# Optimization experiments

Hardware: AMD Instinct MI355X
Metric: run time of the kernel (lower is better)

The kernel has to match this reference:

```python
import jax, jax.numpy as jnp
import numpy as np


def _chamfer(src, tgt):
    # src: [B, N, 3], tgt: [B, M, 3]
    x2 = jnp.sum(src * src, axis=-1)              # [B, N]
    y2 = jnp.sum(tgt * tgt, axis=-1)              # [B, M]
    xy = jnp.einsum('bnd,bmd->bnm', src, tgt)     # [B, N, M]
    d2 = x2[:, :, None] + y2[:, None, :] - 2.0 * xy
    d2 = jnp.maximum(d2, 0.0)                     # guard tiny negatives
    cham_x = jnp.min(d2, axis=2)                  # [B, N] min over tgt
    cham_y = jnp.min(d2, axis=1)                  # [B, M] min over src
    # point_reduction='mean', batch_reduction='sum'
    loss = jnp.sum(jnp.mean(cham_x, axis=1)) + jnp.sum(jnp.mean(cham_y, axis=1))
    return loss


def setup_inputs() -> dict:
    key = jax.random.key(0)
    k1, k2 = jax.random.split(key)
    src = jax.random.normal(k1, (16, 4096, 3), dtype=jnp.float32)
    tgt = jax.random.normal(k2, (16, 4096, 3), dtype=jnp.float32)
    return {"src": src, "tgt": tgt}


def reference(src, tgt):
    wgeo = 1.0
    return wgeo * _chamfer(src, tgt)
```

## Files before the change

kernel.cpp:

```cpp
#include <hip/hip_runtime.h>
#include <hip/hip_bf16.h>


#define BATCH   16
#define NPTS    4096
#define NSTRIPS 32
#define NH      2
#define COLS_PB 2048
#define CHUNKC  512
#define NCHUNKS (COLS_PB / CHUNKC)
#define NSTEP   (CHUNKC / 64)

typedef __attribute__((ext_vector_type(8)))  short short8;
typedef __attribute__((ext_vector_type(16))) float float16;

union U4S8 { uint4 u; short8 s; };

__device__ inline unsigned int bfb(float v) {
    __hip_bfloat16 h = __float2bfloat16(v);
    unsigned short u; __builtin_memcpy(&u, &h, 2);
    return (unsigned int)u;
}
__device__ inline float bff(float v) { return __bfloat162float(__float2bfloat16(v)); }

#define ONEB 0x3F80u

__device__ inline void buildA(float x, float y, float z, uint4& w0, uint4& w1) {
    float xhf = bff(x), yhf = bff(y), zhf = bff(z);
    float f = fmaf(x, x, fmaf(y, y, z * z));
    float fhf = bff(f);
    unsigned xh = bfb(xhf), yh = bfb(yhf), zh = bfb(zhf);
    unsigned xl = bfb(x - xhf), yl = bfb(y - yhf), zl = bfb(z - zhf);
    unsigned fh = bfb(fhf), fl = bfb(f - fhf);
    w0 = make_uint4(xh | (yh << 16), zh | (xh << 16),
                    yh | (zh << 16), xl | (yl << 16));
    w1 = make_uint4(zl | (fh << 16), fl | (ONEB << 16), ONEB, 0u);
}

__device__ inline void buildB(float x, float y, float z, uint4& w0, uint4& w1) {
    float xhf = bff(x), yhf = bff(y), zhf = bff(z);
    float f = fmaf(x, x, fmaf(y, y, z * z));
    float fhf = bff(f);
    unsigned a = bfb(-2.0f * xhf), b = bfb(-2.0f * yhf), c = bfb(-2.0f * zhf);
    unsigned d = bfb(-2.0f * (x - xhf)), e = bfb(-2.0f * (y - yhf)),
             g = bfb(-2.0f * (z - zhf));
    unsigned fh = bfb(fhf), fl = bfb(f - fhf);
    w0 = make_uint4(a | (b << 16), c | (d << 16),
                    e | (g << 16), a | (b << 16));
    w1 = make_uint4(c | (ONEB << 16), ONEB | (fh << 16), fl, 0u);
}

__device__ inline float tree16(const float16& a) {
    float m0 = fminf(fminf(a[0],  a[1]),  a[2]);
    float m1 = fminf(fminf(a[3],  a[4]),  a[5]);
    float m2 = fminf(fminf(a[6],  a[7]),  a[8]);
    float m3 = fminf(fminf(a[9],  a[10]), a[11]);
    float m4 = fminf(fminf(a[12], a[13]), a[14]);
    float p0 = fminf(fminf(m0, m1), a[15]);
    float p1 = fminf(fminf(m2, m3), m4);
    return fminf(p0, p1);
}

__global__ __launch_bounds__(256, 4) void chamfer_main(
    const float* __restrict__ src, const float* __restrict__ tgt,
    unsigned* __restrict__ wsC, unsigned* __restrict__ wsR)
{
    __shared__ uint4 sbuf[2][2][CHUNKC];
    __shared__ unsigned colpart[COLS_PB];

    int blk = blockIdx.x;
    const int strip = blk & (NSTRIPS - 1); blk >>= 5;
    const int b     = blk & 15;            blk >>= 4;
    const int q     = blk;
    const int qoff  = q * COLS_PB;

    const int t    = threadIdx.x;
    const int lane = t & 63;
    const int w    = t >> 6;
    const int h    = lane >> 5;
    const int l5   = lane & 31;

    const float* Araw = src + (size_t)b * NPTS * 3;
    const float* Braw = tgt + (size_t)b * NPTS * 3;

    short8 afr;
    {
        int row = strip * 128 + w * 32 + l5;
        uint4 w0, w1;
        buildA(Araw[3 * row], Araw[3 * row + 1], Araw[3 * row + 2], w0, w1);
        U4S8 tt; tt.u = h ? w1 : w0;
        afr = tt.s;
    }

#pragma unroll
    for (int i = 0; i < COLS_PB / 256; i++) colpart[t + i * 256] = 0xFFFFFFFFu;

    float nx[2][3];
    auto loadRaw = [&](int c) {
#pragma unroll
        for (int k = 0; k < 2; k++) {
            int p = qoff + c * CHUNKC + t + k * 256;
            nx[k][0] = Braw[3 * p + 0];
            nx[k][1] = Braw[3 * p + 1];
            nx[k][2] = Braw[3 * p + 2];
        }
    };
    auto convertWrite = [&](int bi) {
#pragma unroll
        for (int k = 0; k < 2; k++) {
            int lp = t + k * 256;
            uint4 w0, w1;
            buildB(nx[k][0], nx[k][1], nx[k][2], w0, w1);
            sbuf[bi][0][lp] = w0;
            sbuf[bi][1][lp] = w1;
        }
    };

    const float16 z16 = {0.f,0.f,0.f,0.f,0.f,0.f,0.f,0.f,
                         0.f,0.f,0.f,0.f,0.f,0.f,0.f,0.f};
    float rm[16];
#pragma unroll
    for (int r = 0; r < 16; r++) rm[r] = 1e30f;

    loadRaw(0);
    convertWrite(0);
    for (int c = 0; c < NCHUNKS; c++) {
        __syncthreads();
        if (c + 1 < NCHUNKS) loadRaw(c + 1);
        const int bi = c & 1;

        U4S8 c0, c1, n0, n1;
        c0.u = sbuf[bi][h][l5];
        c1.u = sbuf[bi][h][32 + l5];
#pragma unroll 4
        for (int j2 = 0; j2 < NSTEP; j2++) {
            int nj = (j2 + 1) & (NSTEP - 1);
            n0.u = sbuf[bi][h][nj * 64 + l5];
            n1.u = sbuf[bi][h][nj * 64 + 32 + l5];
            float16 a0 = __builtin_amdgcn_mfma_f32_32x32x16_bf16(afr, c0.s, z16, 0, 0, 0);
            float16 a1 = __builtin_amdgcn_mfma_f32_32x32x16_bf16(afr, c1.s, z16, 0, 0, 0);
#pragma unroll
            for (int r = 0; r < 16; r++)
                rm[r] = fminf(fminf(a0[r], a1[r]), rm[r]);
            float cm0 = tree16(a0);
            float cm1 = tree16(a1);
            const int col = c * CHUNKC + j2 * 64 + l5;
            atomicMin(&colpart[col],      __float_as_uint(fmaxf(cm0, 0.0f)));
            atomicMin(&colpart[col + 32], __float_as_uint(fmaxf(cm1, 0.0f)));
            c0 = n0; c1 = n1;
        }
        if (c + 1 < NCHUNKS) convertWrite((c + 1) & 1);
    }

    __syncthreads();
#pragma unroll
    for (int i = 0; i < COLS_PB / 256; i++) {
        const int idx = t + i * 256;
        atomicMin(&wsC[(size_t)b * NPTS + qoff + idx], colpart[idx]);
    }

#pragma unroll
    for (int mask = 1; mask <= 16; mask <<= 1)
#pragma unroll
        for (int r = 0; r < 16; r++)
            rm[r] = fminf(rm[r], __shfl_xor(rm[r], mask, 64));

    __syncthreads();
    if (l5 == 0) {
#pragma unroll
        for (int r = 0; r < 16; r++) {
            const int row = w * 32 + (r & 3) + 8 * (r >> 2) + 4 * h;
            colpart[row] = __float_as_uint(fmaxf(rm[r], 0.0f));
        }
    }
    __syncthreads();
    if (t < 128)
        atomicMin(&wsR[(size_t)b * NPTS + strip * 128 + t], colpart[t]);
}

__global__ __launch_bounds__(256) void finish_reduce(
    const unsigned* __restrict__ wsC, const unsigned* __restrict__ wsR,
    float* __restrict__ out)
{
    __shared__ float wsum[4];
    const int b = blockIdx.x;
    float v = 0.0f;
#pragma unroll
    for (int i = 0; i < 16; i++)
        v += __uint_as_float(wsC[(size_t)b * NPTS + threadIdx.x + i * 256]);
#pragma unroll
    for (int i = 0; i < 16; i++)
        v += __uint_as_float(wsR[(size_t)b * NPTS + threadIdx.x + i * 256]);
#pragma unroll
    for (int mask = 1; mask <= 32; mask <<= 1) v += __shfl_xor(v, mask, 64);
    if ((threadIdx.x & 63) == 0) wsum[threadIdx.x >> 6] = v;
    __syncthreads();
    if (threadIdx.x == 0)
        atomicAdd(out, (wsum[0] + wsum[1] + wsum[2] + wsum[3]) * (1.0f / (float)NPTS));
}

extern "C" void kernel_launch(void* const* d_in, const int* in_sizes, int n_in,
                              void* d_out, int out_size, void* d_ws, size_t ws_size,
                              hipStream_t stream)
{
    const float* src = (const float*)d_in[0];
    const float* tgt = (const float*)d_in[1];
    float* out = (float*)d_out;
    unsigned* wsC = (unsigned*)d_ws;
    unsigned* wsR = wsC + (size_t)BATCH * NPTS;

    hipMemsetAsync(out, 0, sizeof(float), stream);
    hipMemsetAsync(d_ws, 0xFF, (size_t)2 * BATCH * NPTS * sizeof(unsigned), stream);
    chamfer_main <<<NH * BATCH * NSTRIPS, 256, 0, stream>>>(src, tgt, wsC, wsR);
    finish_reduce<<<BATCH, 256, 0, stream>>>(wsC, wsR, out);
}
```

Baseline: 78.67 us.

## Tile two row groups per wave and drop chunked pipeline and output memset

Each block now covers 256 source rows (two A fragments per wave) against 1024 target columns loaded into LDS in one step. Each B fragment read from LDS feeds four MFMAs instead of two, and the column minimum is merged across both row groups before each LDS atomic, halving column atomics per MFMA. The chunked double-buffered staging loop is removed. The finish kernel becomes a single 1024-thread block that writes the output directly, so the output memset and global atomicAdd go away. The trade-offs are more accumulator registers, fewer blocks (1024 rather than 1024, same count but different shape), and a serial single-block final reduction.

```diff
diff --git a/kernel.cpp b/kernel.cpp
--- a/kernel.cpp
+++ b/kernel.cpp
@@ -4,12 +4,10 @@
 
 #define BATCH   16
 #define NPTS    4096
-#define NSTRIPS 32
-#define NH      2
-#define COLS_PB 2048
-#define CHUNKC  512
-#define NCHUNKS (COLS_PB / CHUNKC)
-#define NSTEP   (CHUNKC / 64)
+#define NSTRIPS 16
+#define NQ      4
+#define COLS_PB 1024
+#define NSTEP   (COLS_PB / 64)
 
 typedef __attribute__((ext_vector_type(8)))  short short8;
 typedef __attribute__((ext_vector_type(16))) float float16;
@@ -65,11 +63,11 @@
     const float* __restrict__ src, const float* __restrict__ tgt,
     unsigned* __restrict__ wsC, unsigned* __restrict__ wsR)
 {
-    __shared__ uint4 sbuf[2][2][CHUNKC];
+    __shared__ uint4 sbuf[2][COLS_PB];
     __shared__ unsigned colpart[COLS_PB];
 
     int blk = blockIdx.x;
-    const int strip = blk & (NSTRIPS - 1); blk >>= 5;
+    const int strip = blk & (NSTRIPS - 1); blk >>= 4;
     const int b     = blk & 15;            blk >>= 4;
     const int q     = blk;
     const int qoff  = q * COLS_PB;
@@ -83,73 +81,78 @@
     const float* Araw = src + (size_t)b * NPTS * 3;
     const float* Braw = tgt + (size_t)b * NPTS * 3;
 
-    short8 afr;
-    {
-        int row = strip * 128 + w * 32 + l5;
+    float nx[4][3];
+#pragma unroll
+    for (int k = 0; k < 4; k++) {
+        int p = qoff + t + k * 256;
+        nx[k][0] = Braw[3 * p + 0];
+        nx[k][1] = Braw[3 * p + 1];
+        nx[k][2] = Braw[3 * p + 2];
+    }
+
+    short8 afr[2];
+#pragma unroll
+    for (int g = 0; g < 2; g++) {
+        int row = strip * 256 + g * 128 + w * 32 + l5;
         uint4 w0, w1;
         buildA(Araw[3 * row], Araw[3 * row + 1], Araw[3 * row + 2], w0, w1);
         U4S8 tt; tt.u = h ? w1 : w0;
-        afr = tt.s;
+        afr[g] = tt.s;
     }
 
 #pragma unroll
     for (int i = 0; i < COLS_PB / 256; i++) colpart[t + i * 256] = 0xFFFFFFFFu;
 
-    float nx[2][3];
-    auto loadRaw = [&](int c) {
-#pragma unroll
-        for (int k = 0; k < 2; k++) {
-            int p = qoff + c * CHUNKC + t + k * 256;
-            nx[k][0] = Braw[3 * p + 0];
-            nx[k][1] = Braw[3 * p + 1];
-            nx[k][2] = Braw[3 * p + 2];
-        }
-    };
-    auto convertWrite = [&](int bi) {
-#pragma unroll
-        for (int k = 0; k < 2; k++) {
-            int lp = t + k * 256;
-            uint4 w0, w1;
-            buildB(nx[k][0], nx[k][1], nx[k][2], w0, w1);
-            sbuf[bi][0][lp] = w0;
-            sbuf[bi][1][lp] = w1;
-        }
-    };
+#pragma unroll
+    for (int k = 0; k < 4; k++) {
+        int lp = t + k * 256;
+        uint4 w0, w1;
+        buildB(nx[k][0], nx[k][1], nx[k][2], w0, w1);
+        sbuf[0][lp] = w0;
+        sbuf[1][lp] = w1;
+    }
+    __syncthreads();
 
     const float16 z16 = {0.f,0.f,0.f,0.f,0.f,0.f,0.f,0.f,
                          0.f,0.f,0.f,0.f,0.f,0.f,0.f,0.f};
-    float rm[16];
-#pragma unroll
-    for (int r = 0; r < 16; r++) rm[r] = 1e30f;
-
-    loadRaw(0);
-    convertWrite(0);
-    for (int c = 0; c < NCHUNKS; c++) {
-        __syncthreads();
-        if (c + 1 < NCHUNKS) loadRaw(c + 1);
-        const int bi = c & 1;
-
-        U4S8 c0, c1, n0, n1;
-        c0.u = sbuf[bi][h][l5];
-        c1.u = sbuf[bi][h][32 + l5];
+    float rm[2][16];
+#pragma unroll
+    for (int g = 0; g < 2; g++)
+#pragma unroll
+        for (int r = 0; r < 16; r++) rm[g][r] = 1e30f;
+
+    U4S8 c0, c1, n0, n1;
+    c0.u = sbuf[h][l5];
+    c1.u = sbuf[h][32 + l5];
 #pragma unroll 4
-        for (int j2 = 0; j2 < NSTEP; j2++) {
-            int nj = (j2 + 1) & (NSTEP - 1);
-            n0.u = sbuf[bi][h][nj * 64 + l5];
-            n1.u = sbuf[bi][h][nj * 64 + 32 + l5];
-            float16 a0 = __builtin_amdgcn_mfma_f32_32x32x16_bf16(afr, c0.s, z16, 0, 0, 0);
-            float16 a1 = __builtin_amdgcn_mfma_f32_32x32x16_bf16(afr, c1.s, z16, 0, 0, 0);
+    for (int j = 0; j < NSTEP; j++) {
+        int nj = (j + 1) & (NSTEP - 1);
+        n0.u = sbuf[h][nj * 64 + l5];
+        n1.u = sbuf[h][nj * 64 + 32 + l5];
+
+        float t0, t1;
+        {
+            float16 a0 = __builtin_amdgcn_mfma_f32_32x32x16_bf16(afr[0], c0.s, z16, 0, 0, 0);
+            float16 a1 = __builtin_amdgcn_mfma_f32_32x32x16_bf16(afr[0], c1.s, z16, 0, 0, 0);
 #pragma unroll
             for (int r = 0; r < 16; r++)
-                rm[r] = fminf(fminf(a0[r], a1[r]), rm[r]);
-            float cm0 = tree16(a0);
-            float cm1 = tree16(a1);
-            const int col = c * CHUNKC + j2 * 64 + l5;
-            atomicMin(&colpart[col],      __float_as_uint(fmaxf(cm0, 0.0f)));
-            atomicMin(&colpart[col + 32], __float_as_uint(fmaxf(cm1, 0.0f)));
-            c0 = n0; c1 = n1;
+                rm[0][r] = fminf(fminf(a0[r], a1[r]), rm[0][r]);
+            t0 = tree16(a0);
+            t1 = tree16(a1);
         }
-        if (c + 1 < NCHUNKS) convertWrite((c + 1) & 1);
+        {
+            float16 a0 = __builtin_amdgcn_mfma_f32_32x32x16_bf16(afr[1], c0.s, z16, 0, 0, 0);
+            float16 a1 = __builtin_amdgcn_mfma_f32_32x32x16_bf16(afr[1], c1.s, z16, 0, 0, 0);
+#pragma unroll
+            for (int r = 0; r < 16; r++)
+                rm[1][r] = fminf(fminf(a0[r], a1[r]), rm[1][r]);
+            t0 = fminf(t0, tree16(a0));
+            t1 = fminf(t1, tree16(a1));
+        }
+        const int col = j * 64 + l5;
+        atomicMin(&colpart[col],      __float_as_uint(fmaxf(t0, 0.0f)));
+        atomicMin(&colpart[col + 32], __float_as_uint(fmaxf(t1, 0.0f)));
+        c0 = n0; c1 = n1;
     }
 
     __syncthreads();
@@ -162,41 +165,44 @@
 #pragma unroll
     for (int mask = 1; mask <= 16; mask <<= 1)
 #pragma unroll
-        for (int r = 0; r < 16; r++)
-            rm[r] = fminf(rm[r], __shfl_xor(rm[r], mask, 64));
+        for (int g = 0; g < 2; g++)
+#pragma unroll
+            for (int r = 0; r < 16; r++)
+                rm[g][r] = fminf(rm[g][r], __shfl_xor(rm[g][r], mask, 64));
 
     __syncthreads();
     if (l5 == 0) {
 #pragma unroll
-        for (int r = 0; r < 16; r++) {
-            const int row = w * 32 + (r & 3) + 8 * (r >> 2) + 4 * h;
-            colpart[row] = __float_as_uint(fmaxf(rm[r], 0.0f));
-        }
-    }
-    __syncthreads();
-    if (t < 128)
-        atomicMin(&wsR[(size_t)b * NPTS + strip * 128 + t], colpart[t]);
-}
-
-__global__ __launch_bounds__(256) void finish_reduce(
-    const unsigned* __restrict__ wsC, const unsigned* __restrict__ wsR,
-    float* __restrict__ out)
+        for (int g = 0; g < 2; g++)
+#pragma unroll
+            for (int r = 0; r < 16; r++) {
+                const int row = g * 128 + w * 32 + (r & 3) + 8 * (r >> 2) + 4 * h;
+                colpart[row] = __float_as_uint(fmaxf(rm[g][r], 0.0f));
+            }
+    }
+    __syncthreads();
+    atomicMin(&wsR[(size_t)b * NPTS + strip * 256 + t], colpart[t]);
+}
+
+__global__ __launch_bounds__(1024) void finish_reduce(
+    const unsigned* __restrict__ ws, float* __restrict__ out)
 {
-    __shared__ float wsum[4];
-    const int b = blockIdx.x;
+    __shared__ float wsum[16];
+    const int t = threadIdx.x;
     float v = 0.0f;
 #pragma unroll
-    for (int i = 0; i < 16; i++)
-        v += __uint_as_float(wsC[(size_t)b * NPTS + threadIdx.x + i * 256]);
-#pragma unroll
-    for (int i = 0; i < 16; i++)
-        v += __uint_as_float(wsR[(size_t)b * NPTS + threadIdx.x + i * 256]);
+    for (int i = 0; i < 2 * BATCH * NPTS / 1024; i++)
+        v += __uint_as_float(ws[t + i * 1024]);
 #pragma unroll
     for (int mask = 1; mask <= 32; mask <<= 1) v += __shfl_xor(v, mask, 64);
-    if ((threadIdx.x & 63) == 0) wsum[threadIdx.x >> 6] = v;
-    __syncthreads();
-    if (threadIdx.x == 0)
-        atomicAdd(out, (wsum[0] + wsum[1] + wsum[2] + wsum[3]) * (1.0f / (float)NPTS));
+    if ((t & 63) == 0) wsum[t >> 6] = v;
+    __syncthreads();
+    if (t < 64) {
+        float s = (t < 16) ? wsum[t] : 0.0f;
+#pragma unroll
+        for (int mask = 1; mask <= 8; mask <<= 1) s += __shfl_xor(s, mask, 64);
+        if (t == 0) out[0] = s * (1.0f / (float)NPTS);
+    }
 }
 
 extern "C" void kernel_launch(void* const* d_in, const int* in_sizes, int n_in,
@@ -209,8 +215,7 @@
     unsigned* wsC = (unsigned*)d_ws;
     unsigned* wsR = wsC + (size_t)BATCH * NPTS;
 
-    hipMemsetAsync(out, 0, sizeof(float), stream);
     hipMemsetAsync(d_ws, 0xFF, (size_t)2 * BATCH * NPTS * sizeof(unsigned), stream);
-    chamfer_main <<<NH * BATCH * NSTRIPS, 256, 0, stream>>>(src, tgt, wsC, wsR);
-    finish_reduce<<<BATCH, 256, 0, stream>>>(wsC, wsR, out);
-}
+    chamfer_main <<<NQ * BATCH * NSTRIPS, 256, 0, stream>>>(src, tgt, wsC, wsR);
+    finish_reduce<<<1, 1024, 0, stream>>>(wsC, out);
+}
```

Result: slower. 113.7 us (+44.5%).

## Cut LDS atomics via cross-half shuffle; use LDS transpose for row-min; widen finish grid

Applied to the files above, without the earlier changes.

In the inner loop, the two wave halves now combine their column minima with one cross-lane shuffle, and only half the lanes issue the shared-memory atomicMin, halving the LDS atomic traffic. The row-min epilogue replaces the 5-round shuffle butterfly over 16 registers with a write to a swizzled shared buffer (reusing sbuf) followed by a 32-element scan per row. The finish kernel now uses 32 blocks that each stride over the whole workspace instead of 16 blocks, one per batch. The cost is extra shuffles in the hot loop and idle lanes during the atomics.

```diff
diff --git a/kernel.cpp b/kernel.cpp
--- a/kernel.cpp
+++ b/kernel.cpp
@@ -5,7 +5,7 @@
 #define BATCH   16
 #define NPTS    4096
 #define NSTRIPS 32
-#define NH      2
+#define NQ      2
 #define COLS_PB 2048
 #define CHUNKC  512
 #define NCHUNKS (COLS_PB / CHUNKC)
@@ -65,7 +65,7 @@
     const float* __restrict__ src, const float* __restrict__ tgt,
     unsigned* __restrict__ wsC, unsigned* __restrict__ wsR)
 {
-    __shared__ uint4 sbuf[2][2][CHUNKC];
+    __shared__ uint4    sbuf[2][2][CHUNKC];
     __shared__ unsigned colpart[COLS_PB];
 
     int blk = blockIdx.x;
@@ -133,8 +133,8 @@
         c0.u = sbuf[bi][h][l5];
         c1.u = sbuf[bi][h][32 + l5];
 #pragma unroll 4
-        for (int j2 = 0; j2 < NSTEP; j2++) {
-            int nj = (j2 + 1) & (NSTEP - 1);
+        for (int j = 0; j < NSTEP; j++) {
+            int nj = (j + 1) & (NSTEP - 1);
             n0.u = sbuf[bi][h][nj * 64 + l5];
             n1.u = sbuf[bi][h][nj * 64 + 32 + l5];
             float16 a0 = __builtin_amdgcn_mfma_f32_32x32x16_bf16(afr, c0.s, z16, 0, 0, 0);
@@ -144,53 +144,53 @@
                 rm[r] = fminf(fminf(a0[r], a1[r]), rm[r]);
             float cm0 = tree16(a0);
             float cm1 = tree16(a1);
-            const int col = c * CHUNKC + j2 * 64 + l5;
-            atomicMin(&colpart[col],      __float_as_uint(fmaxf(cm0, 0.0f)));
-            atomicMin(&colpart[col + 32], __float_as_uint(fmaxf(cm1, 0.0f)));
+            cm0 = fminf(cm0, __shfl_xor(cm0, 32, 64));
+            cm1 = fminf(cm1, __shfl_xor(cm1, 32, 64));
+            if (h == 0) {
+                const int col = c * CHUNKC + j * 64 + l5;
+                atomicMin(&colpart[col],      __float_as_uint(fmaxf(cm0, 0.0f)));
+                atomicMin(&colpart[col + 32], __float_as_uint(fmaxf(cm1, 0.0f)));
+            }
             c0 = n0; c1 = n1;
         }
         if (c + 1 < NCHUNKS) convertWrite((c + 1) & 1);
     }
 
     __syncthreads();
+
 #pragma unroll
     for (int i = 0; i < COLS_PB / 256; i++) {
         const int idx = t + i * 256;
         atomicMin(&wsC[(size_t)b * NPTS + qoff + idx], colpart[idx]);
     }
 
-#pragma unroll
-    for (int mask = 1; mask <= 16; mask <<= 1)
-#pragma unroll
-        for (int r = 0; r < 16; r++)
-            rm[r] = fminf(rm[r], __shfl_xor(rm[r], mask, 64));
-
+    float* rowbuf = (float*)&sbuf[0][0][0];
+#pragma unroll
+    for (int r = 0; r < 16; r++) {
+        const int rl = (r & 3) + 8 * (r >> 2) + 4 * h;
+        rowbuf[(w * 32 + rl) * 32 + (l5 ^ rl)] = rm[r];
+    }
     __syncthreads();
-    if (l5 == 0) {
-#pragma unroll
-        for (int r = 0; r < 16; r++) {
-            const int row = w * 32 + (r & 3) + 8 * (r >> 2) + 4 * h;
-            colpart[row] = __float_as_uint(fmaxf(rm[r], 0.0f));
-        }
-    }
-    __syncthreads();
-    if (t < 128)
-        atomicMin(&wsR[(size_t)b * NPTS + strip * 128 + t], colpart[t]);
+    if (t < 128) {
+        const int rl = t & 31;
+        float m = 1e30f;
+#pragma unroll
+        for (int cc = 0; cc < 32; cc++)
+            m = fminf(m, rowbuf[t * 32 + (cc ^ rl)]);
+        atomicMin(&wsR[(size_t)b * NPTS + strip * 128 + t],
+                  __float_as_uint(fmaxf(m, 0.0f)));
+    }
 }
 
 __global__ __launch_bounds__(256) void finish_reduce(
-    const unsigned* __restrict__ wsC, const unsigned* __restrict__ wsR,
-    float* __restrict__ out)
+    const unsigned* __restrict__ ws, float* __restrict__ out)
 {
     __shared__ float wsum[4];
-    const int b = blockIdx.x;
+    const int tg = blockIdx.x * 256 + threadIdx.x;
     float v = 0.0f;
 #pragma unroll
     for (int i = 0; i < 16; i++)
-        v += __uint_as_float(wsC[(size_t)b * NPTS + threadIdx.x + i * 256]);
-#pragma unroll
-    for (int i = 0; i < 16; i++)
-        v += __uint_as_float(wsR[(size_t)b * NPTS + threadIdx.x + i * 256]);
+        v += __uint_as_float(ws[tg + i * 8192]);
 #pragma unroll
     for (int mask = 1; mask <= 32; mask <<= 1) v += __shfl_xor(v, mask, 64);
     if ((threadIdx.x & 63) == 0) wsum[threadIdx.x >> 6] = v;
@@ -211,6 +211,6 @@
 
     hipMemsetAsync(out, 0, sizeof(float), stream);
     hipMemsetAsync(d_ws, 0xFF, (size_t)2 * BATCH * NPTS * sizeof(unsigned), stream);
-    chamfer_main <<<NH * BATCH * NSTRIPS, 256, 0, stream>>>(src, tgt, wsC, wsR);
-    finish_reduce<<<BATCH, 256, 0, stream>>>(wsC, wsR, out);
-}
+    chamfer_main <<<NQ * BATCH * NSTRIPS, 256, 0, stream>>>(src, tgt, wsC, wsR);
+    finish_reduce<<<32, 256, 0, stream>>>((const unsigned*)d_ws, out);
+}
```

Result: slower. 216.1 us (+174.7%).

## Replace global atomicMin partials with plain stores and strip-wise final reduction

Applied to the files above, without the earlier changes.

Each block now writes its per-strip column minima and per-half row minima to private workspace slots with plain stores instead of global atomicMin. The memset of the workspace is dropped. finish_reduce runs 8x more blocks, each reducing the 32 strip partials per column and the 2 row partials. This removes global atomic contention and the memset launch, at the cost of a larger workspace (about 8 MB of column partials) that the finisher must read back.

```diff
diff --git a/kernel.cpp b/kernel.cpp
--- a/kernel.cpp
+++ b/kernel.cpp
@@ -5,7 +5,7 @@
 #define BATCH   16
 #define NPTS    4096
 #define NSTRIPS 32
-#define NH      2
+#define NQ      2
 #define COLS_PB 2048
 #define CHUNKC  512
 #define NCHUNKS (COLS_PB / CHUNKC)
@@ -65,7 +65,7 @@
     const float* __restrict__ src, const float* __restrict__ tgt,
     unsigned* __restrict__ wsC, unsigned* __restrict__ wsR)
 {
-    __shared__ uint4 sbuf[2][2][CHUNKC];
+    __shared__ uint4    sbuf[2][2][CHUNKC];
     __shared__ unsigned colpart[COLS_PB];
 
     int blk = blockIdx.x;
@@ -133,8 +133,8 @@
         c0.u = sbuf[bi][h][l5];
         c1.u = sbuf[bi][h][32 + l5];
 #pragma unroll 4
-        for (int j2 = 0; j2 < NSTEP; j2++) {
-            int nj = (j2 + 1) & (NSTEP - 1);
+        for (int j = 0; j < NSTEP; j++) {
+            int nj = (j + 1) & (NSTEP - 1);
             n0.u = sbuf[bi][h][nj * 64 + l5];
             n1.u = sbuf[bi][h][nj * 64 + 32 + l5];
             float16 a0 = __builtin_amdgcn_mfma_f32_32x32x16_bf16(afr, c0.s, z16, 0, 0, 0);
@@ -144,7 +144,7 @@
                 rm[r] = fminf(fminf(a0[r], a1[r]), rm[r]);
             float cm0 = tree16(a0);
             float cm1 = tree16(a1);
-            const int col = c * CHUNKC + j2 * 64 + l5;
+            const int col = c * CHUNKC + j * 64 + l5;
             atomicMin(&colpart[col],      __float_as_uint(fmaxf(cm0, 0.0f)));
             atomicMin(&colpart[col + 32], __float_as_uint(fmaxf(cm1, 0.0f)));
             c0 = n0; c1 = n1;
@@ -153,10 +153,12 @@
     }
 
     __syncthreads();
-#pragma unroll
-    for (int i = 0; i < COLS_PB / 256; i++) {
-        const int idx = t + i * 256;
-        atomicMin(&wsC[(size_t)b * NPTS + qoff + idx], colpart[idx]);
+
+    {
+        unsigned* cdst = wsC + ((size_t)b * NSTRIPS + strip) * NPTS + qoff;
+#pragma unroll
+        for (int i = 0; i < COLS_PB / 256; i++)
+            cdst[t + i * 256] = colpart[t + i * 256];
     }
 
 #pragma unroll
@@ -175,7 +177,7 @@
     }
     __syncthreads();
     if (t < 128)
-        atomicMin(&wsR[(size_t)b * NPTS + strip * 128 + t], colpart[t]);
+        wsR[((size_t)q * BATCH + b) * NPTS + strip * 128 + t] = colpart[t];
 }
 
 __global__ __launch_bounds__(256) void finish_reduce(
@@ -183,19 +185,29 @@
     float* __restrict__ out)
 {
     __shared__ float wsum[4];
-    const int b = blockIdx.x;
+    const int b   = blockIdx.x >> 3;
+    const int seg = blockIdx.x & 7;
+    const int t   = threadIdx.x;
+
     float v = 0.0f;
 #pragma unroll
-    for (int i = 0; i < 16; i++)
-        v += __uint_as_float(wsC[(size_t)b * NPTS + threadIdx.x + i * 256]);
-#pragma unroll
-    for (int i = 0; i < 16; i++)
-        v += __uint_as_float(wsR[(size_t)b * NPTS + threadIdx.x + i * 256]);
+    for (int cc = 0; cc < 2; cc++) {
+        const int idx = seg * 512 + cc * 256 + t;
+        const unsigned* base = wsC + (size_t)b * NSTRIPS * NPTS + idx;
+        unsigned m = base[0];
+#pragma unroll 8
+        for (int s = 1; s < NSTRIPS; s++) m = min(m, base[(size_t)s * NPTS]);
+        v += __uint_as_float(m);
+        unsigned r = min(wsR[((size_t)0 * BATCH + b) * NPTS + idx],
+                         wsR[((size_t)1 * BATCH + b) * NPTS + idx]);
+        v += __uint_as_float(r);
+    }
+
 #pragma unroll
     for (int mask = 1; mask <= 32; mask <<= 1) v += __shfl_xor(v, mask, 64);
-    if ((threadIdx.x & 63) == 0) wsum[threadIdx.x >> 6] = v;
-    __syncthreads();
-    if (threadIdx.x == 0)
+    if ((t & 63) == 0) wsum[t >> 6] = v;
+    __syncthreads();
+    if (t == 0)
         atomicAdd(out, (wsum[0] + wsum[1] + wsum[2] + wsum[3]) * (1.0f / (float)NPTS));
 }
 
@@ -206,11 +218,11 @@
     const float* src = (const float*)d_in[0];
     const float* tgt = (const float*)d_in[1];
     float* out = (float*)d_out;
+
     unsigned* wsC = (unsigned*)d_ws;
-    unsigned* wsR = wsC + (size_t)BATCH * NPTS;
+    unsigned* wsR = wsC + (size_t)BATCH * NSTRIPS * NPTS;
 
     hipMemsetAsync(out, 0, sizeof(float), stream);
-    hipMemsetAsync(d_ws, 0xFF, (size_t)2 * BATCH * NPTS * sizeof(unsigned), stream);
-    chamfer_main <<<NH * BATCH * NSTRIPS, 256, 0, stream>>>(src, tgt, wsC, wsR);
-    finish_reduce<<<BATCH, 256, 0, stream>>>(wsC, wsR, out);
-}
+    chamfer_main <<<NQ * BATCH * NSTRIPS, 256, 0, stream>>>(src, tgt, wsC, wsR);
+    finish_reduce<<<BATCH * 8, 256, 0, stream>>>(wsC, wsR, out);
+}
```

Result: slower. 83.36 us (+6.0%).
